# Performance work log

Hardware: AMD Instinct MI355X
Metric: run time of the kernel (lower is better)

Reference implementation:

```python
import jax, jax.numpy as jnp
import numpy as np
from jax import lax

K = 128          # kernel_size / n_fft
HOP = 64         # hop_length
IN_CH = 16
OUT_CH = 16
COND = 128
FREQ = K // 2 + 1  # 65


def hann(n):
    # torch.hann_window default (periodic=True)
    return 0.5 * (1.0 - jnp.cos(2.0 * jnp.pi * jnp.arange(n, dtype=jnp.float32) / n))


def _frame_idx(n_frames):
    return jnp.arange(n_frames)[:, None] * HOP + jnp.arange(K)[None, :]


def stft(x, window):
    # x: (N, T) -> (N, FREQ, frames, 2), matches torch.stft(center=True, return_complex=False)
    pad = K // 2
    xp = jnp.pad(x, ((0, 0), (pad, pad)), mode='reflect')
    n_frames = 1 + (xp.shape[1] - K) // HOP
    frames = xp[:, _frame_idx(n_frames)] * window          # (N, frames, K)
    spec = jnp.fft.rfft(frames, axis=-1)                   # (N, frames, FREQ)
    return jnp.stack([spec.real, spec.imag], axis=-1).transpose(0, 2, 1, 3)


def istft(spec, window, length):
    # spec: (N, FREQ, frames) complex -> (N, length); matches torch.istft(center=True)
    frames = jnp.fft.irfft(spec.transpose(0, 2, 1), n=K, axis=-1) * window  # (N, fr, K)
    n_frames = frames.shape[1]
    out_len = K + (n_frames - 1) * HOP
    idx = _frame_idx(n_frames)
    y = jnp.zeros((frames.shape[0], out_len), frames.dtype).at[:, idx].add(frames)
    wsq = jnp.zeros((out_len,), frames.dtype).at[idx].add(
        jnp.broadcast_to(window ** 2, (n_frames, K)))
    y = y / jnp.maximum(wsq, 1e-11)
    pad = K // 2
    return y[:, pad:pad + length]


def setup_inputs() -> dict:
    key = jax.random.key(0)
    ks = jax.random.split(key, 7)
    B, T = 8, 32768
    x = jax.random.normal(ks[0], (B, IN_CH, T), jnp.float32)
    conditioning = jax.random.normal(ks[1], (B, COND, T), jnp.float32)
    conv1_w = jax.random.normal(ks[2], (2 * COND, COND, K), jnp.float32) * 0.02
    conv1_b = jax.random.normal(ks[3], (2 * COND,), jnp.float32) * 0.02
    conv2_w = jax.random.normal(ks[4], (2 * IN_CH * OUT_CH * FREQ, 2 * COND), jnp.float32) * 0.02
    conv2_b = jax.random.normal(ks[5], (2 * IN_CH * OUT_CH * FREQ,), jnp.float32) * 0.02
    bias = jax.random.normal(ks[6], (1, OUT_CH, 1), jnp.float32)
    return {"x": x, "conditioning": conditioning, "conv1_w": conv1_w,
            "conv1_b": conv1_b, "conv2_w": conv2_w, "conv2_b": conv2_b, "bias": bias}


def reference(x, conditioning, conv1_w, conv1_b, conv2_w, conv2_b, bias):
    B, _, T = x.shape
    window = hann(K)

    # filter_net: strided conv + 1x1 conv
    h = lax.conv_general_dilated(conditioning, conv1_w, window_strides=(HOP,),
                                 padding=[(K // 2, K // 2)],
                                 dimension_numbers=('NCH', 'OIH', 'NCH'))
    h = h + conv1_b[None, :, None]                          # (B, 2*COND, frames)
    f = jnp.einsum('bcf,oc->bof', h, conv2_w) + conv2_b[None, :, None]
    n_frames = f.shape[-1]

    # _reshape_filters: channel index c = ((p*OUT + o)*IN + i)*FREQ + fb, p -> last dim
    f = f.reshape(B, 2, OUT_CH, IN_CH, FREQ, n_frames)
    filters = jnp.moveaxis(f, 1, -1)                        # (B, out, in, FREQ, frames, 2)

    X = stft(x.reshape(B * IN_CH, T), window)               # (B*in, FREQ, frames, 2)
    X = X.reshape(B, IN_CH, FREQ, n_frames, 2)

    # elementwise (real/imag separately) multiply then reduce over in_channels
    Y = jnp.einsum('biftp,boiftp->boftp', X, filters)       # (B, out, FREQ, frames, 2)

    spec = (Y[..., 0] + 1j * Y[..., 1]).reshape(B * OUT_CH, FREQ, n_frames)
    out = istft(spec, window, T).reshape(B, OUT_CH, T)
    return out + bias
```

## Files before the change

kernel.cpp:

```cpp
#include <hip/hip_runtime.h>
#include <math.h>

#define TLEN 32768
#define NFR  513
#define TP   576
#define PI_F 3.14159265358979323846f

typedef unsigned short u16;
typedef unsigned int   u32;
typedef _Float16 h16;
typedef h16  half8  __attribute__((ext_vector_type(8)));
typedef h16  half4  __attribute__((ext_vector_type(4)));
typedef float f32x4 __attribute__((ext_vector_type(4)));

#define OFF_TST  0
#define OFF_TI   9216
#define OFF_B2P  19456
#define OFF_R    35840
#define OFF_HT   4295680
#define OFF_X16  4885504
#define OFF_Y16  9899008
#define OFF_W116 14364160

#define F4(p) (*reinterpret_cast<const float4*>(p))
#define GLDS(gsrc, ldst) __builtin_amdgcn_global_load_lds( \
    (const __attribute__((address_space(1))) void*)(gsrc),  \
    (__attribute__((address_space(3))) void*)(ldst), 16, 0, 0)

__device__ __forceinline__ u16 pkh(float v) { return __builtin_bit_cast(u16, (h16)v); }

__global__ void dfc_tables(float* __restrict__ ws) {
  int tid = threadIdx.x;
  u16* Ts = (u16*)(ws + OFF_TST);
  for (int idx = tid; idx < 144*128; idx += 256) {
    int c = idx >> 7, k = idx & 127;
    float v = 0.0f;
    if (c < 136) {
      int p = c / 68, fb = c - p*68;
      if (fb <= 64) {
        float wk = 0.5f*(1.0f - cosf(2.0f*PI_F*(float)k/128.0f));
        float ang = 2.0f*PI_F*(float)((fb*k) & 127)/128.0f;
        v = (p == 0) ? wk*cosf(ang) : -wk*sinf(ang);
      }
    }
    Ts[idx] = pkh(v);
  }
  u16* Ti = (u16*)(ws + OFF_TI);
  for (int idx = tid; idx < 128*160; idx += 256) {
    int k = idx / 160, c = idx - k*160;
    float v = 0.0f;
    if (c < 136) {
      int p = c / 68, fb = c - p*68;
      if (fb <= 64) {
        float wk = 0.5f*(1.0f - cosf(2.0f*PI_F*(float)k/128.0f));
        float cf = (fb == 0 || fb == 64) ? 1.0f : 2.0f;
        float sc = (1.0f/128.0f)*wk*cf;
        float ang = 2.0f*PI_F*(float)((fb*k) & 127)/128.0f;
        int j = k & 63;
        float w0 = 0.5f*(1.0f - cosf(2.0f*PI_F*(float)j/128.0f));
        float w1 = 0.5f*(1.0f - cosf(2.0f*PI_F*(float)(j+64)/128.0f));
        float inv = 1.0f/fmaxf(w0*w0 + w1*w1, 1e-11f);
        v = ((p == 0) ? sc*cosf(ang) : -sc*sinf(ang)) * inv;
      }
    }
    Ti[idx] = pkh(v);
  }
}

__launch_bounds__(256)
__global__ void dfc_prep_w1(const float* __restrict__ w1, u16* __restrict__ w116) {
  int idx = blockIdx.x*256 + threadIdx.x;
  int k8 = idx & 15, rc = idx >> 4;
  int co = rc & 255, ci = rc >> 8;
  const float* src = w1 + ((size_t)(co*128 + ci)*128 + k8*8);
  float4 a = F4(src), b = F4(src + 4);
  half8 hv;
  hv[0]=(h16)a.x; hv[1]=(h16)a.y; hv[2]=(h16)a.z; hv[3]=(h16)a.w;
  hv[4]=(h16)b.x; hv[5]=(h16)b.y; hv[6]=(h16)b.z; hv[7]=(h16)b.w;
  size_t dst = (size_t)ci*32768 + (k8 >> 3)*16384
             + co*64 + ((((k8 & 7) ^ (co & 7))) << 3);
  *(half8*)((h16*)w116 + dst) = hv;
}

__launch_bounds__(256)
__global__ void dfc_prep_w2(const float* __restrict__ w2, u16* __restrict__ w216) {
  int idx = blockIdx.x*256 + threadIdx.x;
  int cc = idx & 31, r = idx >> 5;
  int fb = r % 65;
  const float* src = w2 + (size_t)r*256 + cc*8;
  float4 a = F4(src), b = F4(src + 4);
  half8 hv;
  hv[0]=(h16)a.x; hv[1]=(h16)a.y; hv[2]=(h16)a.z; hv[3]=(h16)a.w;
  hv[4]=(h16)b.x; hv[5]=(h16)b.y; hv[6]=(h16)b.z; hv[7]=(h16)b.w;
  *(half8*)((h16*)w216 + (size_t)r*256 + ((cc ^ (fb & 7)) << 3)) = hv;
}

__launch_bounds__(256)
__global__ void dfc_prep_b2(const float* __restrict__ b2, u16* __restrict__ b2p) {
  int idx = blockIdx.x*256 + threadIdx.x;
  int fb = idx & 63, r = idx >> 6;
  int p = r & 1, oi = r >> 1, o = oi >> 4, i = oi & 15;
  ((h16*)b2p)[idx] = (h16)b2[(size_t)((p*16 + o)*16 + i)*65 + fb];
}

__launch_bounds__(512, 2)
__global__ void dfc_conv1(const float* __restrict__ cond, const u16* __restrict__ w116,
                          u16* __restrict__ hpart) {
  extern __shared__ __align__(16) char LDS[];
  const int flat = (blockIdx.z*8 + blockIdx.y)*9 + blockIdx.x;
  const int kc = flat & 7;
  const int rest = flat >> 3;
  const int b = rest / 9, tile = rest - b*9;
  const int t0 = tile*64;
  const int tid = threadIdx.x;
  const int wave = tid >> 6, lane = tid & 63;
  const int l15 = lane & 15, g16 = lane >> 4;
  const int gbase = t0*64 - 64;
  const bool edge = (tile == 0) || (tile == 8);
  const char* wbB = (const char*)w116 + (size_t)kc*16*65536;
  const float* condB = cond + (size_t)(b*128 + kc*16)*TLEN;

  float4 rv[3];
  auto loadB = [&](int ci) {
    const float* cb = condB + (size_t)ci*TLEN;
    if (!edge) {
      rv[0] = F4(cb + gbase + 4*tid);
      rv[1] = F4(cb + gbase + 4*(512 + tid));
      rv[2] = F4(cb + gbase + 4*(1024 + (tid & 15)));
    } else {
      #pragma unroll
      for (int r = 0; r < 3; ++r) {
        int q = (r < 2) ? (r*512 + tid) : (1024 + (tid & 15));
        int g0 = gbase + 4*q;
        float4 v;
        v.x = (g0   >= 0 && g0   < TLEN) ? cb[g0]   : 0.f;
        v.y = (g0+1 >= 0 && g0+1 < TLEN) ? cb[g0+1] : 0.f;
        v.z = (g0+2 >= 0 && g0+2 < TLEN) ? cb[g0+2] : 0.f;
        v.w = (g0+3 >= 0 && g0+3 < TLEN) ? cb[g0+3] : 0.f;
        rv[r] = v;
      }
    }
  };
  auto writeB = [&](int bslot) {
    u32* seg = (u32*)(LDS + 98304 + bslot*8448);
    #pragma unroll
    for (int r = 0; r < 3; ++r) {
      if (r < 2 || tid < 16) {
        int q = (r < 2) ? (r*512 + tid) : (1024 + tid);
        int s2 = 2*q;
        int ph = s2 ^ (((s2 >> 5) & 7) << 2);
        uint2 pr;
        pr.x = (u32)pkh(rv[r].x) | ((u32)pkh(rv[r].y) << 16);
        pr.y = (u32)pkh(rv[r].z) | ((u32)pkh(rv[r].w) << 16);
        *reinterpret_cast<uint2*>(&seg[ph]) = pr;
      }
    }
  };
  auto stageA = [&](int p, int slot) {
    const char* src = wbB + (size_t)(p >> 1)*65536 + (p & 1)*32768 + wave*4096 + lane*16;
    char* dst = LDS + slot*32768 + wave*4096;
    GLDS(src,        dst);
    GLDS(src + 1024, dst + 1024);
    GLDS(src + 2048, dst + 2048);
    GLDS(src + 3072, dst + 3072);
  };

  loadB(0);
  stageA(0, 0); stageA(1, 1);
  if (edge) asm volatile("s_waitcnt vmcnt(0)" ::: "memory");
  else      asm volatile("s_waitcnt vmcnt(8)" ::: "memory");
  writeB(0);
  loadB(1);

  f32x4 acc[2][4] = {};
  for (int p = 0; p < 32; ++p) {
    const int ci = p >> 1, h = p & 1, sl = p % 3;
    if (edge || p >= 30) asm volatile("s_waitcnt vmcnt(0)" ::: "memory");
    else                 asm volatile("s_waitcnt vmcnt(7)" ::: "memory");
    asm volatile("s_waitcnt lgkmcnt(0)" ::: "memory");
    __builtin_amdgcn_s_barrier();
    __builtin_amdgcn_sched_barrier(0);
    if (p + 2 < 32) stageA(p + 2, (p + 2) % 3);
    if (h == 0 && ci + 1 < 16) {
      if (edge) asm volatile("s_waitcnt vmcnt(0)" ::: "memory");
      else      asm volatile("s_waitcnt vmcnt(4)" ::: "memory");
      writeB((ci + 1) & 1);
      if (ci + 2 < 16) loadB(ci + 2);
    }
    const char* Ab = LDS + sl*32768;
    const u32* seg = (const u32*)(LDS + 98304 + (ci & 1)*8448);
    __builtin_amdgcn_s_setprio(1);
    #pragma unroll
    for (int ks = 0; ks < 2; ++ks) {
      half8 Bf[4];
      #pragma unroll
      for (int nt = 0; nt < 4; ++nt) {
        int s2 = 32*(nt*16 + l15) + 32*h + 16*ks + 4*g16;
        int ph = s2 ^ (((s2 >> 5) & 7) << 2);
        Bf[nt] = *(const half8*)&seg[ph];
      }
      #pragma unroll
      for (int mi = 0; mi < 2; ++mi) {
        int co = wave*32 + mi*16 + l15;
        half8 Af = *(const half8*)(Ab + co*128 + (((ks*4 + g16) ^ (co & 7)) << 4));
        #pragma unroll
        for (int nt = 0; nt < 4; ++nt)
          acc[mi][nt] = __builtin_amdgcn_mfma_f32_16x16x32_f16(Af, Bf[nt], acc[mi][nt], 0,0,0);
      }
    }
    __builtin_amdgcn_s_setprio(0);
  }
  h16* hp = (h16*)hpart;
  #pragma unroll
  for (int mi = 0; mi < 2; ++mi) {
    const int co0 = wave*32 + mi*16 + g16*4;
    #pragma unroll
    for (int nt = 0; nt < 4; ++nt) {
      int t = t0 + nt*16 + l15;
      if (t < NFR) {
        half4 v;
        v[0]=(h16)acc[mi][nt][0]; v[1]=(h16)acc[mi][nt][1];
        v[2]=(h16)acc[mi][nt][2]; v[3]=(h16)acc[mi][nt][3];
        *(half4*)(hp + ((size_t)(kc*8 + b)*NFR + t)*256 + co0) = v;
      }
    }
  }
}

__launch_bounds__(256)
__global__ void dfc_hred(const u16* __restrict__ hpart, const float* __restrict__ b1,
                         u16* __restrict__ hT16) {
  int idx = blockIdx.x*256 + threadIdx.x;
  int b = idx / 16416, r = idx % 16416;
  int t = r >> 5, cc = r & 31;
  float s[8];
  float4 ba = F4(&b1[cc*8]), bb = F4(&b1[cc*8 + 4]);
  s[0]=ba.x; s[1]=ba.y; s[2]=ba.z; s[3]=ba.w; s[4]=bb.x; s[5]=bb.y; s[6]=bb.z; s[7]=bb.w;
  const h16* hp = (const h16*)hpart;
  #pragma unroll
  for (int kc = 0; kc < 8; ++kc) {
    half8 hv = *(const half8*)(hp + ((size_t)(kc*8 + b)*NFR + t)*256 + cc*8);
    #pragma unroll
    for (int j = 0; j < 8; ++j) s[j] += (float)hv[j];
  }
  half8 o;
  #pragma unroll
  for (int j = 0; j < 8; ++j) o[j] = (h16)s[j];
  *(half8*)((h16*)hT16 + ((size_t)b*TP + t)*256 + ((cc ^ (t & 7)) << 3)) = o;
}

__launch_bounds__(256)
__global__ void dfc_stft(const float* __restrict__ x, const float* __restrict__ wsp,
                         u16* __restrict__ X16) {
  __shared__ __align__(16) u32 winu[3104];
  const int tile = blockIdx.x, row = blockIdx.y;
  const int t0 = (tile < 5) ? tile*96 : 417;
  const int tid = threadIdx.x;
  const int wave = tid >> 6, lane = tid & 63;
  const int wm = wave >> 1, wn = wave & 1;
  const int l15 = lane & 15, g16 = lane >> 4;
  const int gbase = t0*64 - 64;
  const bool edge = (tile == 0) || (tile == 5);
  const float* xb = x + (size_t)row*TLEN;

  #pragma unroll
  for (int r = 0; r < 7; ++r) {
    if (r < 6 || tid < 16) {
      int q = (r < 6) ? (tid + 256*r) : (1536 + tid);
      float4 v;
      if (!edge) {
        v = F4(xb + gbase + 4*q);
      } else {
        int g0 = gbase + 4*q;
        float e[4];
        #pragma unroll
        for (int j = 0; j < 4; ++j) {
          int g = g0 + j;
          int sidx = (g < 0) ? -g : ((g >= TLEN) ? (2*TLEN - 2 - g) : g);
          e[j] = xb[sidx];
        }
        v.x = e[0]; v.y = e[1]; v.z = e[2]; v.w = e[3];
      }
      int s2 = 2*q;
      int ph = s2 ^ (((s2 >> 5) & 7) << 2);
      uint2 pr;
      pr.x = (u32)pkh(v.x) | ((u32)pkh(v.y) << 16);
      pr.y = (u32)pkh(v.z) | ((u32)pkh(v.w) << 16);
      *reinterpret_cast<uint2*>(&winu[ph]) = pr;
    }
  }
  __syncthreads();
  const h16* Ts = (const h16*)(wsp + OFF_TST);
  f32x4 acc[5][3] = {};
  #pragma unroll
  for (int ks = 0; ks < 4; ++ks) {
    half8 Bf[3];
    #pragma unroll
    for (int nt = 0; nt < 3; ++nt) {
      int tl = (wn*3 + nt)*16 + l15;
      int s2 = 32*tl + 16*ks + 4*g16;
      int ph = s2 ^ (((s2 >> 5) & 7) << 2);
      Bf[nt] = *(const half8*)&winu[ph];
    }
    #pragma unroll
    for (int m = 0; m < 5; ++m) {
      int mi = wm*4 + m;
      half8 Af = *(const half8*)(Ts + (size_t)(mi*16 + l15)*128 + ks*32 + g16*8);
      #pragma unroll
      for (int nt = 0; nt < 3; ++nt)
        acc[m][nt] = __builtin_amdgcn_mfma_f32_16x16x32_f16(Af, Bf[nt], acc[m][nt], 0,0,0);
    }
  }
  h16* Xh = (h16*)X16;
  #pragma unroll
  for (int m = 0; m < 5; ++m) {
    int c0 = (wm*4 + m)*16 + g16*4;
    if (c0 < 136) {
      #pragma unroll
      for (int nt = 0; nt < 3; ++nt) {
        int t = t0 + (wn*3 + nt)*16 + l15;
        half4 v;
        v[0]=(h16)acc[m][nt][0]; v[1]=(h16)acc[m][nt][1];
        v[2]=(h16)acc[m][nt][2]; v[3]=(h16)acc[m][nt][3];
        *(half4*)(Xh + ((size_t)row*TP + t)*136 + c0) = v;
      }
    }
  }
}

__launch_bounds__(256, 2)
__global__ void dfc_conv2y(const u16* __restrict__ w216, const u16* __restrict__ hT16,
                           const u16* __restrict__ b2p, const u16* __restrict__ X16,
                           u16* __restrict__ Y16) {
  __shared__ __align__(16) char Al[4][16384];
  const int flat = (blockIdx.z*16 + blockIdx.y)*6 + blockIdx.x;
  const int b  = flat & 7;
  const int r2 = flat >> 3;
  const int o  = r2 / 6;
  const int t0 = (r2 - o*6) * 96;
  const int tid = threadIdx.x;
  const int wave = tid >> 6, lane = tid & 63;
  const int wp = wave >> 1, wn = wave & 1;
  const int l15 = lane & 15, g16 = lane >> 4;
  const int lrow8 = lane >> 3, lcol = (lane & 7)*16;
  const char* wb = (const char*)w216;

  half8 Breg[3][8];
  #pragma unroll
  for (int nt = 0; nt < 3; ++nt) {
    int t = t0 + wn*48 + nt*16 + l15;
    const h16* hrow = (const h16*)hT16 + ((size_t)b*TP + t)*256;
    #pragma unroll
    for (int ks = 0; ks < 8; ++ks)
      Breg[nt][ks] = *(const half8*)(hrow + (((ks*4 + g16) ^ (t & 7)) << 3));
  }

  auto stageA = [&](int s, char* dst) {
    const int i = s >> 2, kk = s & 3;
    const int rb0 = (o*16 + i)*65, rb1 = (256 + o*16 + i)*65;
    #pragma unroll
    for (int j = 0; j < 4; ++j) {
      int rr = wave*32 + j*8 + lrow8;
      int wrow = (rr < 64) ? (rb0 + rr) : (rb1 + (rr - 64));
      GLDS(wb + (((size_t)wrow*256 + kk*64) << 1) + lcol, dst + (wave*32 + j*8)*128);
    }
  };

  stageA(0, Al[0]);
  stageA(1, Al[1]);
  __syncthreads();

  f32x4 yac[4][3] = {};
  f32x4 fac[4][3];
  const h16* b2ph = (const h16*)b2p;
  for (int i = 0; i < 16; ++i) {
    #pragma unroll
    for (int mi = 0; mi < 4; ++mi) {
      half4 bh = *(const half4*)(b2ph + (size_t)((o*16 + i)*2 + wp)*64 + mi*16 + g16*4);
      #pragma unroll
      for (int nt = 0; nt < 3; ++nt) {
        fac[mi][nt][0] = (float)bh[0]; fac[mi][nt][1] = (float)bh[1];
        fac[mi][nt][2] = (float)bh[2]; fac[mi][nt][3] = (float)bh[3];
      }
    }
    #pragma unroll
    for (int kk = 0; kk < 4; ++kk) {
      const int s = i*4 + kk;
      if (s < 62) stageA(s + 2, Al[(kk + 2) & 3]);
      if (s < 62)      { asm volatile("s_waitcnt vmcnt(8)" ::: "memory"); }
      else if (s == 62){ asm volatile("s_waitcnt vmcnt(4)" ::: "memory"); }
      else             { asm volatile("s_waitcnt vmcnt(0)" ::: "memory"); }
      __builtin_amdgcn_s_barrier();
      __builtin_amdgcn_sched_barrier(0);
      const char* Ab = Al[kk];
      __builtin_amdgcn_s_setprio(1);
      #pragma unroll
      for (int ks2 = 0; ks2 < 2; ++ks2) {
        half8 Af[4];
        #pragma unroll
        for (int mi = 0; mi < 4; ++mi) {
          int rr = wp*64 + mi*16 + l15;
          Af[mi] = *(const half8*)(Ab + rr*128 + (((ks2*4 + g16) ^ (rr & 7)) << 4));
        }
        #pragma unroll
        for (int mi = 0; mi < 4; ++mi)
          #pragma unroll
          for (int nt = 0; nt < 3; ++nt)
            fac[mi][nt] = __builtin_amdgcn_mfma_f32_16x16x32_f16(Af[mi], Breg[nt][kk*2 + ks2], fac[mi][nt], 0,0,0);
      }
      __builtin_amdgcn_s_setprio(0);
    }
    const h16* Xrow = (const h16*)X16 + (size_t)(b*16 + i)*TP*136;
    #pragma unroll
    for (int mi = 0; mi < 4; ++mi) {
      int fb0 = mi*16 + g16*4;
      #pragma unroll
      for (int nt = 0; nt < 3; ++nt) {
        int t = t0 + wn*48 + nt*16 + l15;
        half4 xv = *(const half4*)(Xrow + (size_t)t*136 + wp*68 + fb0);
        yac[mi][nt][0] += fac[mi][nt][0]*(float)xv[0];
        yac[mi][nt][1] += fac[mi][nt][1]*(float)xv[1];
        yac[mi][nt][2] += fac[mi][nt][2]*(float)xv[2];
        yac[mi][nt][3] += fac[mi][nt][3]*(float)xv[3];
      }
    }
  }
  h16* Yh = (h16*)Y16;
  #pragma unroll
  for (int mi = 0; mi < 4; ++mi) {
    int fb0 = mi*16 + g16*4;
    #pragma unroll
    for (int nt = 0; nt < 3; ++nt) {
      int t = t0 + wn*48 + nt*16 + l15;
      if (t < NFR) {
        half4 v;
        v[0]=(h16)yac[mi][nt][0]; v[1]=(h16)yac[mi][nt][1];
        v[2]=(h16)yac[mi][nt][2]; v[3]=(h16)yac[mi][nt][3];
        *(half4*)(Yh + ((size_t)(b*16 + o)*NFR + t)*136 + wp*68 + fb0) = v;
      }
    }
  }
}

__launch_bounds__(256)
__global__ void dfc_edge(const float* __restrict__ w2, const float* __restrict__ b2,
                         const u16* __restrict__ hT16, const u16* __restrict__ X16,
                         u16* __restrict__ Y16) {
  __shared__ float Wl[8192];
  __shared__ float b2l[32];
  const int o = blockIdx.x, b = blockIdx.y, tc = blockIdx.z, tid = threadIdx.x;
  for (int idx = tid; idx < 8192; idx += 256) {
    int pi = idx >> 8, c = idx & 255;
    int p = pi >> 4, i = pi & 15;
    Wl[idx] = w2[(size_t)(((p*16 + o)*16 + i)*65 + 64)*256 + c];
  }
  if (tid < 32) {
    int p = tid >> 4, i = tid & 15;
    b2l[tid] = b2[(size_t)((p*16 + o)*16 + i)*65 + 64];
  }
  __syncthreads();
  const h16* hh = (const h16*)hT16;
  const h16* Xh = (const h16*)X16;
  h16* Yh = (h16*)Y16;
  for (int t = tc*256 + tid; t < NFR; t += 512) {
    int key = t & 7;
    float facc[32];
    #pragma unroll
    for (int pi = 0; pi < 32; ++pi) facc[pi] = b2l[pi];
    const h16* hrow = hh + ((size_t)b*TP + t)*256;
    for (int cc = 0; cc < 32; ++cc) {
      half8 hv = *(const half8*)(hrow + ((cc ^ key) << 3));
      float h0=(float)hv[0], h1=(float)hv[1], h2=(float)hv[2], h3=(float)hv[3];
      float h4=(float)hv[4], h5=(float)hv[5], h6=(float)hv[6], h7=(float)hv[7];
      #pragma unroll
      for (int pi = 0; pi < 32; ++pi) {
        const float* wr = &Wl[pi*256 + cc*8];
        facc[pi] += wr[0]*h0 + wr[1]*h1 + wr[2]*h2 + wr[3]*h3
                  + wr[4]*h4 + wr[5]*h5 + wr[6]*h6 + wr[7]*h7;
      }
    }
    float y0 = 0.f, y1 = 0.f;
    #pragma unroll
    for (int pi = 0; pi < 32; ++pi) {
      int p = pi >> 4, i = pi & 15;
      float xv = (float)Xh[((size_t)(b*16 + i)*TP + t)*136 + p*68 + 64];
      if (p == 0) y0 += facc[pi]*xv; else y1 += facc[pi]*xv;
    }
    Yh[((size_t)(b*16 + o)*NFR + t)*136 + 0*68 + 64] = (h16)y0;
    Yh[((size_t)(b*16 + o)*NFR + t)*136 + 1*68 + 64] = (h16)y1;
  }
}

__launch_bounds__(256)
__global__ void dfc_istft(const u16* __restrict__ Y16, const float* __restrict__ wsp,
                          const float* __restrict__ bias, float* __restrict__ out) {
  __shared__ __align__(16) char YL[80*336];
  const int u = blockIdx.x, row = blockIdx.y, tid = threadIdx.x;
  const int wave = tid >> 6, lane = tid & 63;
  const int l15 = lane & 15, g16 = lane >> 4;
  for (int i = tid; i < 1680; i += 256) ((float4*)YL)[i] = float4{0.f,0.f,0.f,0.f};
  __syncthreads();
  const char* Yb = (const char*)Y16 + ((size_t)row*NFR + u*64)*272;
  for (int ch = tid; ch < 1105; ch += 256) {
    int tl = ch / 17, cc = ch - tl*17;
    float4 v = F4(Yb + (size_t)tl*272 + cc*16);
    *(float4*)(YL + tl*336 + cc*16) = v;
  }
  __syncthreads();
  const h16* Ti = (const h16*)(wsp + OFF_TI);
  f32x4 acc[2][5] = {};
  #pragma unroll
  for (int ks = 0; ks < 5; ++ks) {
    half8 Af[2];
    #pragma unroll
    for (int m = 0; m < 2; ++m)
      Af[m] = *(const half8*)(Ti + (size_t)((wave*2 + m)*16 + l15)*160 + ks*32 + g16*8);
    #pragma unroll
    for (int nt = 0; nt < 5; ++nt) {
      half8 Bf = *(const half8*)(YL + (nt*16 + l15)*336 + ks*64 + g16*16);
      acc[0][nt] = __builtin_amdgcn_mfma_f32_16x16x32_f16(Af[0], Bf, acc[0][nt], 0,0,0);
      acc[1][nt] = __builtin_amdgcn_mfma_f32_16x16x32_f16(Af[1], Bf, acc[1][nt], 0,0,0);
    }
  }
  __syncthreads();
  float* outT = (float*)YL;
  if (wave >= 2) {
    #pragma unroll
    for (int m = 0; m < 2; ++m) {
      int j0 = (wave*2 + m - 4)*16 + g16*4;
      #pragma unroll
      for (int nt = 0; nt < 4; ++nt) {
        int t = nt*16 + l15;
        *(f32x4*)&outT[t*68 + j0] = acc[m][nt];
      }
    }
  }
  __syncthreads();
  if (wave < 2) {
    #pragma unroll
    for (int m = 0; m < 2; ++m) {
      int j0 = (wave*2 + m)*16 + g16*4;
      #pragma unroll
      for (int nt = 0; nt < 5; ++nt) {
        int t = nt*16 + l15;
        if (t >= 1 && t <= 64) {
          f32x4 v = *(f32x4*)&outT[(t-1)*68 + j0];
          v[0] += acc[m][nt][0]; v[1] += acc[m][nt][1];
          v[2] += acc[m][nt][2]; v[3] += acc[m][nt][3];
          *(f32x4*)&outT[(t-1)*68 + j0] = v;
        }
      }
    }
  }
  __syncthreads();
  const float bv = bias[row & 15];
  float* og = out + (size_t)row*TLEN + (size_t)u*4096;
  #pragma unroll
  for (int r = 0; r < 4; ++r) {
    int fi = tid + 256*r;
    int sg = fi >> 4, jj = (fi & 15)*4;
    float4 v = *(float4*)&outT[sg*68 + jj];
    float4 w{v.x + bv, v.y + bv, v.z + bv, v.w + bv};
    *(float4*)(og + sg*64 + jj) = w;
  }
}

extern "C" void kernel_launch(void* const* d_in, const int* in_sizes, int n_in,
                              void* d_out, int out_size, void* d_ws, size_t ws_size,
                              hipStream_t stream) {
  (void)in_sizes; (void)n_in; (void)out_size; (void)ws_size;
  const float* x    = (const float*)d_in[0];
  const float* cond = (const float*)d_in[1];
  const float* w1   = (const float*)d_in[2];
  const float* b1   = (const float*)d_in[3];
  const float* w2   = (const float*)d_in[4];
  const float* b2   = (const float*)d_in[5];
  const float* bias = (const float*)d_in[6];
  float* ws  = (float*)d_ws;
  float* out = (float*)d_out;
  u16* R     = (u16*)(ws + OFF_R);
  u16* b2p   = (u16*)(ws + OFF_B2P);
  u16* hT16  = (u16*)(ws + OFF_HT);
  u16* X16   = (u16*)(ws + OFF_X16);
  u16* Y16   = (u16*)(ws + OFF_Y16);
  u16* w116  = (u16*)(ws + OFF_W116);

  (void)hipMemsetAsync(hT16, 0, (size_t)8*TP*256*2, stream);
  (void)hipMemsetAsync(X16, 0, (size_t)128*TP*136*2, stream);
  dfc_tables<<<dim3(1), dim3(256), 0, stream>>>(ws);
  dfc_prep_w1<<<dim3(2048), dim3(256), 0, stream>>>(w1, w116);
  dfc_conv1<<<dim3(9, 8, 8), dim3(512), 115200, stream>>>(cond, w116, R);
  dfc_hred<<<dim3(513), dim3(256), 0, stream>>>(R, b1, hT16);
  dfc_prep_w2<<<dim3(4160), dim3(256), 0, stream>>>(w2, R);
  dfc_prep_b2<<<dim3(128), dim3(256), 0, stream>>>(b2, b2p);
  dfc_stft<<<dim3(6, 128), dim3(256), 0, stream>>>(x, ws, X16);
  dfc_conv2y<<<dim3(6, 16, 8), dim3(256), 0, stream>>>(R, hT16, b2p, X16, Y16);
  dfc_edge<<<dim3(16, 8, 2), dim3(256), 0, stream>>>(w2, b2, hT16, X16, Y16);
  dfc_istft<<<dim3(8, 128), dim3(256), 0, stream>>>(Y16, ws, bias, out);
}
```

Before: 477.6 us.

## Triple-buffer conv2 weight staging and prefetch X/bias loads early

The conv2y kernel drops from a 4-slot to a 3-slot LDS ring for the weight tiles and raises the launch bound to 3 blocks per CU. X and bias loads for each input channel are issued at the start of the k-loop instead of after the MFMA chain, so their latency overlaps the matrix work. The bias add moves into the final accumulate, and the staging of the next tile is issued after the barrier. The changed vmcnt waits are tuned by hand and may be fragile, and holding the prefetched X/bias values raises register pressure against the tighter occupancy bound.

```diff
diff --git a/kernel.cpp b/kernel.cpp
--- a/kernel.cpp
+++ b/kernel.cpp
@@ -328,11 +328,11 @@
   }
 }
 
-__launch_bounds__(256, 2)
+__launch_bounds__(256, 3)
 __global__ void dfc_conv2y(const u16* __restrict__ w216, const u16* __restrict__ hT16,
                            const u16* __restrict__ b2p, const u16* __restrict__ X16,
                            u16* __restrict__ Y16) {
-  __shared__ __align__(16) char Al[4][16384];
+  __shared__ __align__(16) char Al[3][16384];
   const int flat = (blockIdx.z*16 + blockIdx.y)*6 + blockIdx.x;
   const int b  = flat & 7;
   const int r2 = flat >> 3;
@@ -372,27 +372,42 @@
 
   f32x4 yac[4][3] = {};
   f32x4 fac[4][3];
+  half4 xv[4][3];
+  half4 bh[4];
   const h16* b2ph = (const h16*)b2p;
   for (int i = 0; i < 16; ++i) {
     #pragma unroll
-    for (int mi = 0; mi < 4; ++mi) {
-      half4 bh = *(const half4*)(b2ph + (size_t)((o*16 + i)*2 + wp)*64 + mi*16 + g16*4);
-      #pragma unroll
-      for (int nt = 0; nt < 3; ++nt) {
-        fac[mi][nt][0] = (float)bh[0]; fac[mi][nt][1] = (float)bh[1];
-        fac[mi][nt][2] = (float)bh[2]; fac[mi][nt][3] = (float)bh[3];
-      }
-    }
-    #pragma unroll
     for (int kk = 0; kk < 4; ++kk) {
       const int s = i*4 + kk;
-      if (s < 62) stageA(s + 2, Al[(kk + 2) & 3]);
-      if (s < 62)      { asm volatile("s_waitcnt vmcnt(8)" ::: "memory"); }
-      else if (s == 62){ asm volatile("s_waitcnt vmcnt(4)" ::: "memory"); }
-      else             { asm volatile("s_waitcnt vmcnt(0)" ::: "memory"); }
+      if (kk == 0) {
+        const h16* Xrow = (const h16*)X16 + (size_t)(b*16 + i)*TP*136;
+        #pragma unroll
+        for (int mi = 0; mi < 4; ++mi) {
+          int fb0 = mi*16 + g16*4;
+          #pragma unroll
+          for (int nt = 0; nt < 3; ++nt) {
+            int t = t0 + wn*48 + nt*16 + l15;
+            xv[mi][nt] = *(const half4*)(Xrow + (size_t)t*136 + wp*68 + fb0);
+          }
+          bh[mi] = *(const half4*)(b2ph + (size_t)((o*16 + i)*2 + wp)*64 + fb0);
+        }
+      }
+      __builtin_amdgcn_sched_barrier(0);
+      if (s == 63)     { asm volatile("s_waitcnt vmcnt(0)"  ::: "memory"); }
+      else if (kk >= 2){ asm volatile("s_waitcnt vmcnt(8)"  ::: "memory"); }
+      else             { asm volatile("s_waitcnt vmcnt(24)" ::: "memory"); }
       __builtin_amdgcn_s_barrier();
       __builtin_amdgcn_sched_barrier(0);
-      const char* Ab = Al[kk];
+      if (s + 2 <= 63) stageA(s + 2, Al[(s + 2) % 3]);
+      __builtin_amdgcn_sched_barrier(0);
+      if (kk == 0) {
+        #pragma unroll
+        for (int mi = 0; mi < 4; ++mi)
+          #pragma unroll
+          for (int nt = 0; nt < 3; ++nt)
+            fac[mi][nt] = f32x4{0.f, 0.f, 0.f, 0.f};
+      }
+      const char* Ab = Al[s % 3];
       __builtin_amdgcn_s_setprio(1);
       #pragma unroll
       for (int ks2 = 0; ks2 < 2; ++ks2) {
@@ -409,19 +424,14 @@
             fac[mi][nt] = __builtin_amdgcn_mfma_f32_16x16x32_f16(Af[mi], Breg[nt][kk*2 + ks2], fac[mi][nt], 0,0,0);
       }
       __builtin_amdgcn_s_setprio(0);
-    }
-    const h16* Xrow = (const h16*)X16 + (size_t)(b*16 + i)*TP*136;
-    #pragma unroll
-    for (int mi = 0; mi < 4; ++mi) {
-      int fb0 = mi*16 + g16*4;
-      #pragma unroll
-      for (int nt = 0; nt < 3; ++nt) {
-        int t = t0 + wn*48 + nt*16 + l15;
-        half4 xv = *(const half4*)(Xrow + (size_t)t*136 + wp*68 + fb0);
-        yac[mi][nt][0] += fac[mi][nt][0]*(float)xv[0];
-        yac[mi][nt][1] += fac[mi][nt][1]*(float)xv[1];
-        yac[mi][nt][2] += fac[mi][nt][2]*(float)xv[2];
-        yac[mi][nt][3] += fac[mi][nt][3]*(float)xv[3];
+      if (kk == 3) {
+        #pragma unroll
+        for (int mi = 0; mi < 4; ++mi)
+          #pragma unroll
+          for (int nt = 0; nt < 3; ++nt)
+            #pragma unroll
+            for (int e = 0; e < 4; ++e)
+              yac[mi][nt][e] += (fac[mi][nt][e] + (float)bh[mi][e]) * (float)xv[mi][nt][e];
       }
     }
   }
```

Measured after the change: 646.0 us. 1.35x slower.
